# Kernel tuning notes

Hardware: AMD Instinct MI355X
Metric: run time of the kernel (lower is better)

The kernel has to match this reference:

```python
import jax, jax.numpy as jnp
import numpy as np

A = -0.75  # PyTorch bicubic coefficient
NEG_SLOPE = 0.01  # LeakyReLU default


def _cubic_kernel(s):
    # s: absolute distance, PyTorch cubic convolution kernel with a=-0.75
    s = jnp.abs(s)
    w1 = ((A + 2.0) * s - (A + 3.0)) * s * s + 1.0          # |s| <= 1
    w2 = (((s - 5.0) * s + 8.0) * s - 4.0) * A               # 1 < |s| < 2
    return jnp.where(s <= 1.0, w1, jnp.where(s < 2.0, w2, 0.0))


def _resize_matrix(n_in, n_out):
    """[n_out, n_in] bicubic interpolation matrix, align_corners=True, border-clamped."""
    scale = (n_in - 1) / (n_out - 1)
    src = jnp.arange(n_out, dtype=jnp.float32) * jnp.float32(scale)
    i0 = jnp.floor(src).astype(jnp.int32)
    t = src - i0.astype(jnp.float32)
    offs = jnp.arange(-1, 3)                     # [-1, 0, 1, 2]
    idx = jnp.clip(i0[:, None] + offs[None, :], 0, n_in - 1)   # [n_out, 4]
    w = _cubic_kernel(t[:, None] - offs[None, :].astype(jnp.float32))  # [n_out, 4]
    rows = jnp.broadcast_to(jnp.arange(n_out)[:, None], idx.shape)
    return jnp.zeros((n_out, n_in), dtype=jnp.float32).at[rows, idx].add(w)


def setup_inputs() -> dict:
    key = jax.random.key(0)
    k1, k2, k3 = jax.random.split(key, 3)
    B, C_IN, C_OUT, H, W = 8, 256, 128, 128, 128
    x = jax.random.normal(k1, (B, C_IN, H, W), dtype=jnp.float32)
    weight = jax.random.normal(k2, (C_OUT, C_IN), dtype=jnp.float32) * (1.0 / np.sqrt(C_IN))
    bias = jax.random.normal(k3, (C_OUT,), dtype=jnp.float32) * 0.01
    return {"x": x, "weight": weight, "bias": bias}


def reference(x, weight, bias):
    B, C, H, W = x.shape
    Mh = _resize_matrix(H, 2 * H)   # [2H, H]
    Mw = _resize_matrix(W, 2 * W)   # [2W, W]
    # Separable bicubic upsample: up[b,c,i,j] = sum_hw Mh[i,h] x[b,c,h,w] Mw[j,w]
    up = jnp.einsum('ih,bchw,jw->bcij', Mh, x, Mw)
    # 1x1 conv (per-pixel channel matmul) + bias
    y = jnp.einsum('oc,bcij->boij', weight, up) + bias[None, :, None, None]
    # LeakyReLU(0.01)
    return jnp.where(y >= 0, y, NEG_SLOPE * y)
```

## Files before the change

kernel.cpp:

```cpp
#include <hip/hip_runtime.h>
#include <hip/hip_bf16.h>

#define BB 8
#define CIN 256
#define COUT 128
#define HIN 128
#define WIN 128
#define HOUT 256
#define WOUT 256

typedef __attribute__((ext_vector_type(8))) short bf16x8;
typedef __attribute__((ext_vector_type(4))) float f32x4;

__device__ __forceinline__ short f2bf(float f) {
  __hip_bfloat16 h = __float2bfloat16(f);
  return *reinterpret_cast<short*>(&h);
}
__device__ __forceinline__ float bf2f(short s) {
  unsigned int u = ((unsigned int)(unsigned short)s) << 16;
  return __uint_as_float(u);
}

__global__ __launch_bounds__(256) void wconv_kernel(const float* __restrict__ wgt,
                                                    short* __restrict__ wbf) {
  int idx = (blockIdx.x * 256 + threadIdx.x) * 4;
  float4 f = *reinterpret_cast<const float4*>(wgt + idx);
  short4 pk = make_short4(f2bf(f.x), f2bf(f.y), f2bf(f.z), f2bf(f.w));
  *reinterpret_cast<short4*>(wbf + idx) = pk;
}

__global__ __launch_bounds__(256, 4) void conv1x1_kernel(const float* __restrict__ x,
                                                         const short* __restrict__ wbf,
                                                         short* __restrict__ zbf) {
  __shared__ __align__(16) short smem[128 * 128];
  const int h = blockIdx.x, b = blockIdx.y;
  const int t = threadIdx.x;

  const int lane = t & 63, wid = t >> 6;
  const int wm = wid >> 1, wn = wid & 1;
  const int r = lane & 15, g = lane >> 4;

  f32x4 acc[4][4];
#pragma unroll
  for (int i = 0; i < 4; ++i)
#pragma unroll
    for (int j = 0; j < 4; ++j)
      acc[i][j] = (f32x4){0.f, 0.f, 0.f, 0.f};

  const float* xb = x + (size_t)b * (CIN * HIN * WIN) + (size_t)h * WIN;
  const int w0 = t & 127;
  const int ch = t >> 7;

  for (int ph = 0; ph < 2; ++ph) {
#pragma unroll
    for (int cc = 0; cc < 8; ++cc) {
      int kl = ch * 8 + cc;
      int c = ph * 128 + kl * 8;
      float f[8];
#pragma unroll
      for (int i = 0; i < 8; ++i)
        f[i] = xb[(size_t)(c + i) * (HIN * WIN) + w0];
      bf16x8 pk;
#pragma unroll
      for (int i = 0; i < 8; ++i) pk[i] = f2bf(f[i]);
      *reinterpret_cast<bf16x8*>(&smem[w0 * 128 + ((kl ^ (w0 & 15)) * 8)]) = pk;
    }
    __syncthreads();

#pragma unroll
    for (int ks = 0; ks < 4; ++ks) {
      int kk = ks * 4 + g;
      int kg = ph * 16 + kk;
      bf16x8 xfr[4], wfr[4];
#pragma unroll
      for (int mt = 0; mt < 4; ++mt) {
        int p = wm * 64 + mt * 16 + r;
        xfr[mt] = *reinterpret_cast<const bf16x8*>(&smem[p * 128 + ((kk ^ (p & 15)) * 8)]);
      }
#pragma unroll
      for (int nt = 0; nt < 4; ++nt) {
        int o = wn * 64 + nt * 16 + r;
        wfr[nt] = *reinterpret_cast<const bf16x8*>(wbf + (size_t)o * CIN + kg * 8);
      }
#pragma unroll
      for (int mt = 0; mt < 4; ++mt)
#pragma unroll
        for (int nt = 0; nt < 4; ++nt)
          acc[mt][nt] = __builtin_amdgcn_mfma_f32_16x16x32_bf16(xfr[mt], wfr[nt], acc[mt][nt], 0, 0, 0);
    }
    __syncthreads();
  }

#pragma unroll
  for (int mt = 0; mt < 4; ++mt) {
#pragma unroll
    for (int nt = 0; nt < 4; ++nt) {
      int o = wn * 64 + nt * 16 + r;
      int w4 = wm * 64 + mt * 16 + g * 4;
      int cw = w4 >> 3, sub = w4 & 7;
      short4 pk = make_short4(f2bf(acc[mt][nt][0]), f2bf(acc[mt][nt][1]),
                              f2bf(acc[mt][nt][2]), f2bf(acc[mt][nt][3]));
      *reinterpret_cast<short4*>(&smem[o * 128 + ((cw ^ (o & 15)) << 3) + sub]) = pk;
    }
  }
  __syncthreads();

  short* zb = zbf + (size_t)b * (COUT * HIN * WIN) + (size_t)h * WIN;
  const int ck = t & 15;
#pragma unroll
  for (int p = 0; p < 8; ++p) {
    int ro = p * 16 + (t >> 4);
    bf16x8 v = *reinterpret_cast<const bf16x8*>(&smem[ro * 128 + ((ck ^ (ro & 15)) << 3)]);
    *reinterpret_cast<bf16x8*>(zb + (size_t)ro * (HIN * WIN) + ck * 8) = v;
  }
}

#define ACF (-0.75f)
#define NEG 0.01f

__device__ __forceinline__ float cub_le1(float s) {
  return ((ACF + 2.0f) * s - (ACF + 3.0f)) * s * s + 1.0f;
}
__device__ __forceinline__ float cub_gt1(float s) {
  return (((s - 5.0f) * s + 8.0f) * s - 4.0f) * ACF;
}
__device__ __forceinline__ float4 mkw(float tt) {
  return make_float4(cub_gt1(1.0f + tt), cub_le1(tt), cub_le1(1.0f - tt), cub_gt1(2.0f - tt));
}

__global__ __launch_bounds__(256) void upsample_kernel(const short* __restrict__ zbf,
                                                       const float* __restrict__ bias,
                                                       float* __restrict__ out) {
  __shared__ float zrow[20][128];
  __shared__ float trow[20][256];

  const int bx = blockIdx.x;
  const int itile = bx & 7;
  const int o = bx >> 3;
  const int b = blockIdx.y;
  const int t = threadIdx.x;

  const int m0 = itile * 16;
  const int hmin = max(m0 - 2, 0);
  const int hmax = min(m0 + 15 + 2, HIN - 1);
  const int nh = hmax - hmin + 1;

  {
    const short* zb = zbf + ((size_t)b * COUT + o) * (HIN * WIN);
    for (int q = t; q < nh * 16; q += 256) {
      int hr = q >> 4, c8 = (q & 15) * 8;
      bf16x8 v = *reinterpret_cast<const bf16x8*>(zb + (size_t)(hmin + hr) * WIN + c8);
      float4 lo = make_float4(bf2f(v[0]), bf2f(v[1]), bf2f(v[2]), bf2f(v[3]));
      float4 hi = make_float4(bf2f(v[4]), bf2f(v[5]), bf2f(v[6]), bf2f(v[7]));
      *reinterpret_cast<float4*>(&zrow[hr][c8]) = lo;
      *reinterpret_cast<float4*>(&zrow[hr][c8 + 4]) = hi;
    }
  }
  __syncthreads();

  {
    const int u = t & 127;
    const int pr = t >> 7;
    const float uf = (float)u;
    const float4 wA = mkw((255.0f - uf) * (1.0f / 255.0f));
    const float4 wB = mkw((127.0f - uf) * (1.0f / 255.0f));
    const int i0c = max(u - 2, 0);
    const int i1c = max(u - 1, 0);
    const int i2c = u;
    const int i3c = min(u + 1, WIN - 1);
    const int i4c = min(u + 2, WIN - 1);
    for (int hr = pr; hr < nh; hr += 2) {
      float z0 = zrow[hr][i0c], z1 = zrow[hr][i1c], z2 = zrow[hr][i2c];
      float z3 = zrow[hr][i3c], z4 = zrow[hr][i4c];
      float oa = wA.x * z0 + wA.y * z1 + wA.z * z2 + wA.w * z3;
      float ob = wB.x * z1 + wB.y * z2 + wB.z * z3 + wB.w * z4;
      *reinterpret_cast<float2*>(&trow[hr][u * 2]) = make_float2(oa, ob);
    }
  }
  __syncthreads();

  const float bv = bias[o];
  const int j4 = t & 63;
  const int iw = t >> 6;
  float* obase = out + ((size_t)b * COUT + o) * (HOUT * WOUT);
  for (int mm = iw; mm < 16; mm += 4) {
    int m = m0 + mm;
    float mf = (float)m;
    float4 wA = mkw((255.0f - mf) * (1.0f / 255.0f));
    float4 wB = mkw((127.0f - mf) * (1.0f / 255.0f));
    int r0 = max(m - 2, 0) - hmin;
    int r1 = max(m - 1, 0) - hmin;
    int r2 = m - hmin;
    int r3 = min(m + 1, HIN - 1) - hmin;
    int r4 = min(m + 2, HIN - 1) - hmin;
    float4 t0 = *reinterpret_cast<const float4*>(&trow[r0][j4 * 4]);
    float4 t1 = *reinterpret_cast<const float4*>(&trow[r1][j4 * 4]);
    float4 t2 = *reinterpret_cast<const float4*>(&trow[r2][j4 * 4]);
    float4 t3 = *reinterpret_cast<const float4*>(&trow[r3][j4 * 4]);
    float4 t4 = *reinterpret_cast<const float4*>(&trow[r4][j4 * 4]);
    f32x4 rA, rB;
    rA.x = wA.x * t0.x + wA.y * t1.x + wA.z * t2.x + wA.w * t3.x + bv;
    rA.y = wA.x * t0.y + wA.y * t1.y + wA.z * t2.y + wA.w * t3.y + bv;
    rA.z = wA.x * t0.z + wA.y * t1.z + wA.z * t2.z + wA.w * t3.z + bv;
    rA.w = wA.x * t0.w + wA.y * t1.w + wA.z * t2.w + wA.w * t3.w + bv;
    rB.x = wB.x * t1.x + wB.y * t2.x + wB.z * t3.x + wB.w * t4.x + bv;
    rB.y = wB.x * t1.y + wB.y * t2.y + wB.z * t3.y + wB.w * t4.y + bv;
    rB.z = wB.x * t1.z + wB.y * t2.z + wB.z * t3.z + wB.w * t4.z + bv;
    rB.w = wB.x * t1.w + wB.y * t2.w + wB.z * t3.w + wB.w * t4.w + bv;
    rA.x = rA.x >= 0.f ? rA.x : rA.x * NEG;
    rA.y = rA.y >= 0.f ? rA.y : rA.y * NEG;
    rA.z = rA.z >= 0.f ? rA.z : rA.z * NEG;
    rA.w = rA.w >= 0.f ? rA.w : rA.w * NEG;
    rB.x = rB.x >= 0.f ? rB.x : rB.x * NEG;
    rB.y = rB.y >= 0.f ? rB.y : rB.y * NEG;
    rB.z = rB.z >= 0.f ? rB.z : rB.z * NEG;
    rB.w = rB.w >= 0.f ? rB.w : rB.w * NEG;
    int iA = itile * 32 + 2 * mm;
    __builtin_nontemporal_store(rA, reinterpret_cast<f32x4*>(obase + (size_t)iA * WOUT + j4 * 4));
    __builtin_nontemporal_store(rB, reinterpret_cast<f32x4*>(obase + (size_t)(iA + 1) * WOUT + j4 * 4));
  }
}

extern "C" void kernel_launch(void* const* d_in, const int* in_sizes, int n_in,
                              void* d_out, int out_size, void* d_ws, size_t ws_size,
                              hipStream_t stream) {
  const float* x = (const float*)d_in[0];
  const float* wgt = (const float*)d_in[1];
  const float* bias = (const float*)d_in[2];
  float* out = (float*)d_out;

  short* zbf = (short*)d_ws;
  short* wbf = (short*)((char*)d_ws + (size_t)BB * COUT * HIN * WIN * sizeof(short));

  wconv_kernel<<<dim3(COUT * CIN / (256 * 4)), 256, 0, stream>>>(wgt, wbf);
  conv1x1_kernel<<<dim3(HIN, BB), 256, 0, stream>>>(x, wbf, zbf);
  upsample_kernel<<<dim3(COUT * 8, BB), 256, 0, stream>>>(zbf, bias, out);
}
```

Before: 99.85 us.

## Prefetch second channel half into registers during first-half MFMA in conv1x1

The conv1x1 kernel now issues all 64 global loads for the second half of the input channels into registers before running the MFMA loop on the first half. The conversion to bf16 and the LDS store happen after that loop. This overlaps global memory latency with tensor-core compute instead of load, sync, then compute per phase. The extra 64 live floats per thread raise register pressure, so the launch-bounds occupancy hint drops from 4 to 2 blocks per CU. That trades occupancy-based latency hiding for explicit prefetch.

```diff
diff --git a/kernel.cpp b/kernel.cpp
--- a/kernel.cpp
+++ b/kernel.cpp
@@ -29,7 +29,7 @@
   *reinterpret_cast<short4*>(wbf + idx) = pk;
 }
 
-__global__ __launch_bounds__(256, 4) void conv1x1_kernel(const float* __restrict__ x,
+__global__ __launch_bounds__(256, 2) void conv1x1_kernel(const float* __restrict__ x,
                                                          const short* __restrict__ wbf,
                                                          short* __restrict__ zbf) {
   __shared__ __align__(16) short smem[128 * 128];
@@ -40,56 +40,95 @@
   const int wm = wid >> 1, wn = wid & 1;
   const int r = lane & 15, g = lane >> 4;
 
-  f32x4 acc[4][4];
-#pragma unroll
-  for (int i = 0; i < 4; ++i)
-#pragma unroll
-    for (int j = 0; j < 4; ++j)
-      acc[i][j] = (f32x4){0.f, 0.f, 0.f, 0.f};
-
   const float* xb = x + (size_t)b * (CIN * HIN * WIN) + (size_t)h * WIN;
   const int w0 = t & 127;
   const int ch = t >> 7;
 
-  for (int ph = 0; ph < 2; ++ph) {
-#pragma unroll
-    for (int cc = 0; cc < 8; ++cc) {
-      int kl = ch * 8 + cc;
-      int c = ph * 128 + kl * 8;
-      float f[8];
-#pragma unroll
-      for (int i = 0; i < 8; ++i)
-        f[i] = xb[(size_t)(c + i) * (HIN * WIN) + w0];
-      bf16x8 pk;
-#pragma unroll
-      for (int i = 0; i < 8; ++i) pk[i] = f2bf(f[i]);
-      *reinterpret_cast<bf16x8*>(&smem[w0 * 128 + ((kl ^ (w0 & 15)) * 8)]) = pk;
-    }
-    __syncthreads();
-
-#pragma unroll
-    for (int ks = 0; ks < 4; ++ks) {
-      int kk = ks * 4 + g;
-      int kg = ph * 16 + kk;
-      bf16x8 xfr[4], wfr[4];
-#pragma unroll
-      for (int mt = 0; mt < 4; ++mt) {
-        int p = wm * 64 + mt * 16 + r;
-        xfr[mt] = *reinterpret_cast<const bf16x8*>(&smem[p * 128 + ((kk ^ (p & 15)) * 8)]);
-      }
-#pragma unroll
-      for (int nt = 0; nt < 4; ++nt) {
-        int o = wn * 64 + nt * 16 + r;
-        wfr[nt] = *reinterpret_cast<const bf16x8*>(wbf + (size_t)o * CIN + kg * 8);
-      }
-#pragma unroll
-      for (int mt = 0; mt < 4; ++mt)
-#pragma unroll
-        for (int nt = 0; nt < 4; ++nt)
-          acc[mt][nt] = __builtin_amdgcn_mfma_f32_16x16x32_bf16(xfr[mt], wfr[nt], acc[mt][nt], 0, 0, 0);
-    }
-    __syncthreads();
-  }
+  f32x4 acc[4][4];
+#pragma unroll
+  for (int i = 0; i < 4; ++i)
+#pragma unroll
+    for (int j = 0; j < 4; ++j)
+      acc[i][j] = (f32x4){0.f, 0.f, 0.f, 0.f};
+
+  float f0[64], f1[64];
+
+#pragma unroll
+  for (int cc = 0; cc < 8; ++cc)
+#pragma unroll
+    for (int i = 0; i < 8; ++i)
+      f0[cc * 8 + i] = xb[(size_t)((ch * 8 + cc) * 8 + i) * (HIN * WIN) + w0];
+
+#pragma unroll
+  for (int cc = 0; cc < 8; ++cc) {
+    int kl = ch * 8 + cc;
+    bf16x8 pk;
+#pragma unroll
+    for (int i = 0; i < 8; ++i) pk[i] = f2bf(f0[cc * 8 + i]);
+    *reinterpret_cast<bf16x8*>(&smem[w0 * 128 + ((kl ^ (w0 & 15)) * 8)]) = pk;
+  }
+  __syncthreads();
+
+#pragma unroll
+  for (int cc = 0; cc < 8; ++cc)
+#pragma unroll
+    for (int i = 0; i < 8; ++i)
+      f1[cc * 8 + i] = xb[(size_t)(128 + (ch * 8 + cc) * 8 + i) * (HIN * WIN) + w0];
+
+#pragma unroll
+  for (int ks = 0; ks < 4; ++ks) {
+    int kk = ks * 4 + g;
+    bf16x8 xfr[4], wfr[4];
+#pragma unroll
+    for (int mt = 0; mt < 4; ++mt) {
+      int p = wm * 64 + mt * 16 + r;
+      xfr[mt] = *reinterpret_cast<const bf16x8*>(&smem[p * 128 + ((kk ^ (p & 15)) * 8)]);
+    }
+#pragma unroll
+    for (int nt = 0; nt < 4; ++nt) {
+      int o = wn * 64 + nt * 16 + r;
+      wfr[nt] = *reinterpret_cast<const bf16x8*>(wbf + (size_t)o * CIN + kk * 8);
+    }
+#pragma unroll
+    for (int mt = 0; mt < 4; ++mt)
+#pragma unroll
+      for (int nt = 0; nt < 4; ++nt)
+        acc[mt][nt] = __builtin_amdgcn_mfma_f32_16x16x32_bf16(xfr[mt], wfr[nt], acc[mt][nt], 0, 0, 0);
+  }
+  __syncthreads();
+
+#pragma unroll
+  for (int cc = 0; cc < 8; ++cc) {
+    int kl = ch * 8 + cc;
+    bf16x8 pk;
+#pragma unroll
+    for (int i = 0; i < 8; ++i) pk[i] = f2bf(f1[cc * 8 + i]);
+    *reinterpret_cast<bf16x8*>(&smem[w0 * 128 + ((kl ^ (w0 & 15)) * 8)]) = pk;
+  }
+  __syncthreads();
+
+#pragma unroll
+  for (int ks = 0; ks < 4; ++ks) {
+    int kk = ks * 4 + g;
+    int kg = 16 + kk;
+    bf16x8 xfr[4], wfr[4];
+#pragma unroll
+    for (int mt = 0; mt < 4; ++mt) {
+      int p = wm * 64 + mt * 16 + r;
+      xfr[mt] = *reinterpret_cast<const bf16x8*>(&smem[p * 128 + ((kk ^ (p & 15)) * 8)]);
+    }
+#pragma unroll
+    for (int nt = 0; nt < 4; ++nt) {
+      int o = wn * 64 + nt * 16 + r;
+      wfr[nt] = *reinterpret_cast<const bf16x8*>(wbf + (size_t)o * CIN + kg * 8);
+    }
+#pragma unroll
+    for (int mt = 0; mt < 4; ++mt)
+#pragma unroll
+      for (int nt = 0; nt < 4; ++nt)
+        acc[mt][nt] = __builtin_amdgcn_mfma_f32_16x16x32_bf16(xfr[mt], wfr[nt], acc[mt][nt], 0, 0, 0);
+  }
+  __syncthreads();
 
 #pragma unroll
   for (int mt = 0; mt < 4; ++mt) {
```

Result: faster. 93.99 us (-5.9%).

## Load x fragments directly into registers with double-buffered software pipeline in conv1x1

Applied to the files above, without the earlier changes.

The conv1x1 kernel no longer stages x through shared memory. Each wave loads its MFMA A-fragments straight from global memory into registers, converts them to bf16, and double-buffers the next k-slice's loads while the current slice's MFMAs issue. This removes the LDS staging and its two barriers. Warp tiling changes from 2x2 waves of 64x64 to four waves of 32x128 each. Block-to-row mapping is swizzled and launch bounds drop to 2 blocks/SM, which adds register pressure. The per-lane global loads are 16-lane runs of contiguous floats and may coalesce less well than before.

```diff
diff --git a/kernel.cpp b/kernel.cpp
--- a/kernel.cpp
+++ b/kernel.cpp
@@ -29,74 +29,74 @@
   *reinterpret_cast<short4*>(wbf + idx) = pk;
 }
 
-__global__ __launch_bounds__(256, 4) void conv1x1_kernel(const float* __restrict__ x,
+__global__ __launch_bounds__(256, 2) void conv1x1_kernel(const float* __restrict__ x,
                                                          const short* __restrict__ wbf,
                                                          short* __restrict__ zbf) {
   __shared__ __align__(16) short smem[128 * 128];
-  const int h = blockIdx.x, b = blockIdx.y;
+  const int bx = blockIdx.x, b = blockIdx.y;
+  const int h = ((bx & 7) << 4) + (bx >> 3);
   const int t = threadIdx.x;
 
   const int lane = t & 63, wid = t >> 6;
-  const int wm = wid >> 1, wn = wid & 1;
   const int r = lane & 15, g = lane >> 4;
-
-  f32x4 acc[4][4];
-#pragma unroll
-  for (int i = 0; i < 4; ++i)
-#pragma unroll
-    for (int j = 0; j < 4; ++j)
+  const int wbase = wid * 32;
+
+  const float* xq = x + (size_t)b * (CIN * HIN * WIN) + (size_t)h * WIN
+                    + (size_t)(g * 8) * (HIN * WIN) + wbase + r;
+  const short* wq = wbf + (size_t)r * CIN + g * 8;
+
+  f32x4 acc[2][8];
+#pragma unroll
+  for (int i = 0; i < 2; ++i)
+#pragma unroll
+    for (int j = 0; j < 8; ++j)
       acc[i][j] = (f32x4){0.f, 0.f, 0.f, 0.f};
 
-  const float* xb = x + (size_t)b * (CIN * HIN * WIN) + (size_t)h * WIN;
-  const int w0 = t & 127;
-  const int ch = t >> 7;
-
-  for (int ph = 0; ph < 2; ++ph) {
-#pragma unroll
-    for (int cc = 0; cc < 8; ++cc) {
-      int kl = ch * 8 + cc;
-      int c = ph * 128 + kl * 8;
-      float f[8];
-#pragma unroll
-      for (int i = 0; i < 8; ++i)
-        f[i] = xb[(size_t)(c + i) * (HIN * WIN) + w0];
-      bf16x8 pk;
-#pragma unroll
-      for (int i = 0; i < 8; ++i) pk[i] = f2bf(f[i]);
-      *reinterpret_cast<bf16x8*>(&smem[w0 * 128 + ((kl ^ (w0 & 15)) * 8)]) = pk;
-    }
-    __syncthreads();
-
-#pragma unroll
-    for (int ks = 0; ks < 4; ++ks) {
-      int kk = ks * 4 + g;
-      int kg = ph * 16 + kk;
-      bf16x8 xfr[4], wfr[4];
-#pragma unroll
-      for (int mt = 0; mt < 4; ++mt) {
-        int p = wm * 64 + mt * 16 + r;
-        xfr[mt] = *reinterpret_cast<const bf16x8*>(&smem[p * 128 + ((kk ^ (p & 15)) * 8)]);
-      }
-#pragma unroll
-      for (int nt = 0; nt < 4; ++nt) {
-        int o = wn * 64 + nt * 16 + r;
-        wfr[nt] = *reinterpret_cast<const bf16x8*>(wbf + (size_t)o * CIN + kg * 8);
-      }
-#pragma unroll
-      for (int mt = 0; mt < 4; ++mt)
-#pragma unroll
-        for (int nt = 0; nt < 4; ++nt)
-          acc[mt][nt] = __builtin_amdgcn_mfma_f32_16x16x32_bf16(xfr[mt], wfr[nt], acc[mt][nt], 0, 0, 0);
-    }
-    __syncthreads();
-  }
-
-#pragma unroll
-  for (int mt = 0; mt < 4; ++mt) {
-#pragma unroll
-    for (int nt = 0; nt < 4; ++nt) {
-      int o = wn * 64 + nt * 16 + r;
-      int w4 = wm * 64 + mt * 16 + g * 4;
+  float ra[16], rb[16];
+
+#define LOADK(kk, buf)                                                        \
+  {                                                                           \
+    _Pragma("unroll") for (int mt = 0; mt < 2; ++mt)                          \
+        _Pragma("unroll") for (int i = 0; i < 8; ++i)                         \
+            buf[mt * 8 + i] =                                                 \
+                xq[(size_t)((kk) * 32 + i) * (HIN * WIN) + mt * 16];          \
+  }
+
+#define MFMAK(kk, buf)                                                        \
+  {                                                                           \
+    bf16x8 xfr[2], wfr[8];                                                    \
+    _Pragma("unroll") for (int mt = 0; mt < 2; ++mt) {                        \
+      _Pragma("unroll") for (int i = 0; i < 8; ++i)                           \
+          xfr[mt][i] = f2bf(buf[mt * 8 + i]);                                 \
+    }                                                                         \
+    _Pragma("unroll") for (int nt = 0; nt < 8; ++nt)                          \
+        wfr[nt] = *reinterpret_cast<const bf16x8*>(wq + (size_t)(nt * 16) * CIN + (kk) * 32); \
+    _Pragma("unroll") for (int mt = 0; mt < 2; ++mt)                          \
+        _Pragma("unroll") for (int nt = 0; nt < 8; ++nt)                      \
+            acc[mt][nt] = __builtin_amdgcn_mfma_f32_16x16x32_bf16(            \
+                xfr[mt], wfr[nt], acc[mt][nt], 0, 0, 0);                      \
+  }
+
+  LOADK(0, ra)
+#pragma unroll
+  for (int ks2 = 0; ks2 < 4; ++ks2) {
+    const int k0 = ks2 * 2;
+    LOADK(k0 + 1, rb)
+    MFMAK(k0, ra)
+    if (k0 + 2 < 8) LOADK(k0 + 2, ra)
+    MFMAK(k0 + 1, rb)
+  }
+#undef LOADK
+#undef MFMAK
+
+  __syncthreads();
+
+#pragma unroll
+  for (int mt = 0; mt < 2; ++mt) {
+#pragma unroll
+    for (int nt = 0; nt < 8; ++nt) {
+      int o = nt * 16 + r;
+      int w4 = wbase + mt * 16 + g * 4;
       int cw = w4 >> 3, sub = w4 & 7;
       short4 pk = make_short4(f2bf(acc[mt][nt][0]), f2bf(acc[mt][nt][1]),
                               f2bf(acc[mt][nt][2]), f2bf(acc[mt][nt][3]));
```

Measured after the change: 97.81 us. 2.0% less time.

## Load conv input via direct global-to-LDS fp32 copies and convert on fragment read

Applied to the files above, without the earlier changes.

The 1x1 conv kernel now stages x tiles into shared memory with global_load_lds 16-byte direct copies of fp32 data, 64 channels per phase over 4 phases, instead of per-thread scalar loads, bf16 packing and LDS stores. The fp32-to-bf16 conversion moves to the MFMA fragment read, which now does 8 strided scalar LDS reads per fragment. This cuts register traffic and load instruction count in the staging step, but it adds more LDS read instructions, possible bank conflicts, and more barrier phases.

```diff
diff --git a/kernel.cpp b/kernel.cpp
--- a/kernel.cpp
+++ b/kernel.cpp
@@ -21,6 +21,12 @@
   return __uint_as_float(u);
 }
 
+typedef __attribute__((address_space(3))) unsigned int lds_u32;
+typedef const __attribute__((address_space(1))) unsigned int glb_u32;
+__device__ __forceinline__ void gload16(const float* g, float* l) {
+  __builtin_amdgcn_global_load_lds((glb_u32*)g, (lds_u32*)l, 16, 0, 0);
+}
+
 __global__ __launch_bounds__(256) void wconv_kernel(const float* __restrict__ wgt,
                                                     short* __restrict__ wbf) {
   int idx = (blockIdx.x * 256 + threadIdx.x) * 4;
@@ -32,14 +38,16 @@
 __global__ __launch_bounds__(256, 4) void conv1x1_kernel(const float* __restrict__ x,
                                                          const short* __restrict__ wbf,
                                                          short* __restrict__ zbf) {
-  __shared__ __align__(16) short smem[128 * 128];
+  __shared__ __align__(16) float smemf[64 * 128];
+  short* smems = (short*)smemf;
   const int h = blockIdx.x, b = blockIdx.y;
   const int t = threadIdx.x;
-
   const int lane = t & 63, wid = t >> 6;
   const int wm = wid >> 1, wn = wid & 1;
   const int r = lane & 15, g = lane >> 4;
 
+  const float* xb = x + (size_t)b * (CIN * HIN * WIN) + (size_t)h * WIN;
+
   f32x4 acc[4][4];
 #pragma unroll
   for (int i = 0; i < 4; ++i)
@@ -47,39 +55,35 @@
     for (int j = 0; j < 4; ++j)
       acc[i][j] = (f32x4){0.f, 0.f, 0.f, 0.f};
 
-  const float* xb = x + (size_t)b * (CIN * HIN * WIN) + (size_t)h * WIN;
-  const int w0 = t & 127;
-  const int ch = t >> 7;
-
-  for (int ph = 0; ph < 2; ++ph) {
-#pragma unroll
-    for (int cc = 0; cc < 8; ++cc) {
-      int kl = ch * 8 + cc;
-      int c = ph * 128 + kl * 8;
-      float f[8];
-#pragma unroll
-      for (int i = 0; i < 8; ++i)
-        f[i] = xb[(size_t)(c + i) * (HIN * WIN) + w0];
-      bf16x8 pk;
-#pragma unroll
-      for (int i = 0; i < 8; ++i) pk[i] = f2bf(f[i]);
-      *reinterpret_cast<bf16x8*>(&smem[w0 * 128 + ((kl ^ (w0 & 15)) * 8)]) = pk;
-    }
+  const int lplane = lane >> 5;
+  const int lw4 = (lane & 31) * 4;
+
+  for (int ph = 0; ph < 4; ++ph) {
+    const int cbase = ph * 64 + wid * 16;
+#pragma unroll
+    for (int i = 0; i < 8; ++i) {
+      const float* src = xb + (size_t)(cbase + i * 2 + lplane) * (HIN * WIN) + lw4;
+      float* dst = &smemf[(wid * 16 + i * 2) * 128];
+      gload16(src, dst);
+    }
+    asm volatile("s_waitcnt vmcnt(0)" ::: "memory");
     __syncthreads();
 
 #pragma unroll
-    for (int ks = 0; ks < 4; ++ks) {
-      int kk = ks * 4 + g;
-      int kg = ph * 16 + kk;
+    for (int ks = 0; ks < 2; ++ks) {
+      const int cl0 = ks * 32 + g * 8;
+      const int kg = ph * 8 + ks * 4 + g;
       bf16x8 xfr[4], wfr[4];
 #pragma unroll
       for (int mt = 0; mt < 4; ++mt) {
-        int p = wm * 64 + mt * 16 + r;
-        xfr[mt] = *reinterpret_cast<const bf16x8*>(&smem[p * 128 + ((kk ^ (p & 15)) * 8)]);
+        const int w = wm * 64 + mt * 16 + r;
+#pragma unroll
+        for (int j = 0; j < 8; ++j)
+          xfr[mt][j] = f2bf(smemf[(cl0 + j) * 128 + w]);
       }
 #pragma unroll
       for (int nt = 0; nt < 4; ++nt) {
-        int o = wn * 64 + nt * 16 + r;
+        const int o = wn * 64 + nt * 16 + r;
         wfr[nt] = *reinterpret_cast<const bf16x8*>(wbf + (size_t)o * CIN + kg * 8);
       }
 #pragma unroll
@@ -100,7 +104,7 @@
       int cw = w4 >> 3, sub = w4 & 7;
       short4 pk = make_short4(f2bf(acc[mt][nt][0]), f2bf(acc[mt][nt][1]),
                               f2bf(acc[mt][nt][2]), f2bf(acc[mt][nt][3]));
-      *reinterpret_cast<short4*>(&smem[o * 128 + ((cw ^ (o & 15)) << 3) + sub]) = pk;
+      *reinterpret_cast<short4*>(&smems[o * 128 + ((cw ^ (o & 15)) << 3) + sub]) = pk;
     }
   }
   __syncthreads();
@@ -110,7 +114,7 @@
 #pragma unroll
   for (int p = 0; p < 8; ++p) {
     int ro = p * 16 + (t >> 4);
-    bf16x8 v = *reinterpret_cast<const bf16x8*>(&smem[ro * 128 + ((ck ^ (ro & 15)) << 3)]);
+    bf16x8 v = *reinterpret_cast<const bf16x8*>(&smems[ro * 128 + ((ck ^ (ro & 15)) << 3)]);
     *reinterpret_cast<bf16x8*>(zb + (size_t)ro * (HIN * WIN) + ck * 8) = v;
   }
 }
```

New measurement: 89.06 us (median of 3 runs). -10.8%, faster.
